# Performance work log

Measured on AMD Instinct MI355X. Metric: run time of the kernel, lower is better.

The kernel has to match this reference:

```python
import math
import jax, jax.numpy as jnp
import numpy as np

HIDDEN = 1024
N_HEADS = 16
HEAD = HIDDEN // N_HEADS
B = 2
L = 2048
STRIDE = 128
EXPR = 8
MAXPOS = 2048


def _checkpoint(wi):
    if wi % STRIDE == 0 and wi != 0:
        return wi - EXPR
    return (wi // STRIDE) * STRIDE + STRIDE - EXPR


def _subset_summaries(absolute_max):
    ci = _checkpoint(0)
    s = set()
    while ci <= absolute_max - 1:
        s |= set(range(ci, min(ci + EXPR + 1, absolute_max)))
        ci = _checkpoint(ci + STRIDE)
    return s


def build_sparse_mask(n, bidirectional=True):
    # Faithful numpy port of prepare_sparse_mask: -1e4 everywhere, 0 at allowed positions.
    mask = np.full((n, n), -10000.0, dtype=np.float32)
    global_summaries = _subset_summaries(n) if bidirectional else set()
    for i in range(n):
        absolute_max = n if bidirectional else i + 1
        rounded = ((i + STRIDE) // STRIDE) * STRIDE
        if i % STRIDE == 0 and i != 0:
            s1 = set(range(i - STRIDE, min(absolute_max, i + 1)))
        else:
            s1 = set(range(max(0, rounded - STRIDE), min(absolute_max, rounded + 1)))
        s2 = set() if bidirectional else _subset_summaries(absolute_max)
        idx = sorted(s1 | s2 | global_summaries)
        mask[i, idx] = 0.0
    return mask


def setup_inputs() -> dict:
    key = jax.random.key(0)
    ks = jax.random.split(key, 8)
    s = 1.0 / math.sqrt(HIDDEN)
    inp = {
        "hidden_states": jax.random.normal(ks[0], (B, L, HIDDEN), dtype=jnp.float32),
        "attention_mask": jnp.zeros((B, 1, 1, L), dtype=jnp.float32),
        "Wq": jax.random.normal(ks[1], (HIDDEN, HIDDEN), dtype=jnp.float32) * s,
        "bq": jnp.zeros((HIDDEN,), dtype=jnp.float32),
        "Wk": jax.random.normal(ks[2], (HIDDEN, HIDDEN), dtype=jnp.float32) * s,
        "bk": jnp.zeros((HIDDEN,), dtype=jnp.float32),
        "Wv": jax.random.normal(ks[3], (HIDDEN, HIDDEN), dtype=jnp.float32) * s,
        "bv": jnp.zeros((HIDDEN,), dtype=jnp.float32),
        "sparse_mask": jnp.asarray(build_sparse_mask(MAXPOS)[:L, :L]),
    }
    return inp


def _split_heads(x):  # [B, L, H] -> [B, nH, L, hd]
    b, l, _ = x.shape
    return x.reshape(b, l, N_HEADS, HEAD).transpose(0, 2, 1, 3)


def reference(hidden_states, attention_mask, Wq, bq, Wk, bk, Wv, bv, sparse_mask):
    q = _split_heads(hidden_states @ Wq + bq)
    k = _split_heads(hidden_states @ Wk + bk)
    v = _split_heads(hidden_states @ Wv + bv)
    scores = jnp.einsum("bhqd,bhkd->bhqk", q, k) / math.sqrt(HEAD)
    scores = scores + sparse_mask  # [L,L] broadcasts over [B,nH,L,L]
    scores = jnp.clip(scores, -10000.0, 10000.0)
    scores = scores + attention_mask
    probs = jax.nn.softmax(scores.astype(jnp.float32), axis=-1).astype(scores.dtype)
    # dropout prob = 0.0 -> identity
    ctx = jnp.einsum("bhqk,bhkd->bhqd", probs, v)
    return ctx.transpose(0, 2, 1, 3).reshape(hidden_states.shape[0], -1, HIDDEN)
```

## Files before the change

kernel.cpp:

```cpp
#include <hip/hip_runtime.h>

#define HID 1024
#define NH 16
#define HD 64
#define BB 2
#define LL 2048
#define GC 143
#define GP 192
#define AMT_PER_B 2240

typedef __attribute__((ext_vector_type(8))) __bf16 bf16x8;
typedef __attribute__((ext_vector_type(4))) float f32x4;
typedef __attribute__((ext_vector_type(4))) int i32x4;
typedef __attribute__((ext_vector_type(2))) unsigned long long u64x2;

__device__ __forceinline__ void gload_lds16(const void* g, void* l) {
  __builtin_amdgcn_global_load_lds((const __attribute__((address_space(1))) void*)g,
                                   (__attribute__((address_space(3))) void*)l, 16, 0, 0);
}

__device__ __forceinline__ unsigned int cvtpk(float lo, float hi) {
  unsigned int r;
  asm("v_cvt_pk_bf16_f32 %0, %1, %2" : "=v"(r) : "v"(lo), "v"(hi));
  return r;
}

__device__ __forceinline__ bf16x8 vfrag(const char* vbase, int r, int gA, int gB,
                                        int half) {
  unsigned long long lo =
      *(const unsigned long long*)(vbase + r * 128 + ((gA ^ (r & 7)) << 4) + half);
  unsigned long long hi =
      *(const unsigned long long*)(vbase + r * 128 + ((gB ^ (r & 7)) << 4) + half);
  u64x2 u;
  u[0] = lo;
  u[1] = hi;
  return __builtin_bit_cast(bf16x8, u);
}

__global__ __launch_bounds__(256) void prep_kernel(
    const float* __restrict__ hs, __bf16* __restrict__ hsb,
    const float* __restrict__ Wq, const float* __restrict__ Wk,
    const float* __restrict__ Wv, __bf16* __restrict__ wtb,
    const float* __restrict__ amask, unsigned int* __restrict__ zbase,
    float* __restrict__ amt) {
  int bx = blockIdx.x;
  int t = threadIdx.x;
  if (bx < 2048) {
    int i = bx * 256 + t;
    const float4* src = (const float4*)hs;
    float4 a = src[2 * i], b = src[2 * i + 1];
    bf16x8 v;
    v[0] = (__bf16)a.x; v[1] = (__bf16)a.y; v[2] = (__bf16)a.z; v[3] = (__bf16)a.w;
    v[4] = (__bf16)b.x; v[5] = (__bf16)b.y; v[6] = (__bf16)b.z; v[7] = (__bf16)b.w;
    ((bf16x8*)hsb)[i] = v;
  } else if (bx < 2048 + 768) {
    int z3 = bx - 2048;
    int kt = z3 & 15, nt = (z3 >> 4) & 15, z = z3 >> 8;
    const float* w = (z == 0) ? Wq : (z == 1) ? Wk : Wv;
    __bf16* dst = wtb + (size_t)z * HID * HID;
    __shared__ __bf16 tile[64][66];
    int cr = t & 63, rr = t >> 6;
#pragma unroll
    for (int it = 0; it < 16; it++) {
      int r = it * 4 + rr;
      tile[cr][r] = (__bf16)w[(size_t)(kt * 64 + r) * HID + nt * 64 + cr];
    }
    __syncthreads();
#pragma unroll
    for (int it = 0; it < 16; it++) {
      int r = it * 4 + rr;
      dst[(size_t)(nt * 64 + r) * HID + kt * 64 + cr] = tile[r][cr];
    }
  } else if (bx < 2048 + 768 + 1536) {
    int i = (bx - 2816) * 256 + t;
    zbase[i] = 0u;
  } else {
    int idx = (bx - 4352) * 256 + t;
    if (idx < BB * AMT_PER_B) {
      int b = idx / AMT_PER_B, r = idx % AMT_PER_B;
      float val;
      if (r < GP) {
        int k = r / 9, j = r - 9 * k;
        val = (r < GC) ? (amask[b * LL + 120 + 128 * k + j] - 20.f) : -1e5f;
      } else {
        int r2 = r - GP;
        int w = r2 >> 7, off = r2 & 127;
        bool gcol = (off >= 120) || (off == 0 && w != 0);
        val = gcol ? -1e5f : (amask[b * LL + w * 128 + off] - 20.f);
      }
      amt[idx] = val;
    }
  }
}

__global__ __launch_bounds__(256, 2) void qkv_gemm_kernel(
    const __bf16* __restrict__ hsb, const __bf16* __restrict__ wtb,
    const float* __restrict__ bq, const float* __restrict__ bk,
    const float* __restrict__ bv, __bf16* __restrict__ qb,
    __bf16* __restrict__ kkb, __bf16* __restrict__ vtb,
    __bf16* __restrict__ kgb, __bf16* __restrict__ vgb) {
  int nt = blockIdx.x, mt = blockIdx.y, which = blockIdx.z;
  const __bf16* wt = wtb + (size_t)which * HID * HID;
  const float* bias = (which == 0) ? bq : (which == 1) ? bk : bv;

  __shared__ __bf16 a_lds[128 * 64];
  __shared__ __bf16 b_lds[128 * 64];

  int tid = threadIdx.x;
  int wave = tid >> 6, lane = tid & 63;
  int wm = wave >> 1, wn = wave & 1;
  int lrow = lane & 15, lgr = lane >> 4, g = lane & 7;

  f32x4 acc[4][4];
#pragma unroll
  for (int i = 0; i < 4; i++)
#pragma unroll
    for (int j = 0; j < 4; j++) acc[i][j] = f32x4{0.f, 0.f, 0.f, 0.f};

  for (int kk = 0; kk < HID; kk += 64) {
#pragma unroll
    for (int i = 0; i < 4; i++) {
      int r = (wave * 4 + i) * 8 + (lane >> 3);
      int gs = (g ^ (r & 7)) * 8;
      gload_lds16(hsb + (size_t)(mt * 128 + r) * HID + kk + gs,
                  &a_lds[(wave * 4 + i) * 512]);
      gload_lds16(wt + (size_t)(nt * 128 + r) * HID + kk + gs,
                  &b_lds[(wave * 4 + i) * 512]);
    }
    __syncthreads();
#pragma unroll
    for (int kf = 0; kf < 2; kf++) {
      bf16x8 af[4], bfr[4];
#pragma unroll
      for (int mr = 0; mr < 4; mr++) {
        int row = wm * 64 + mr * 16 + lrow;
        af[mr] = *(const bf16x8*)((const char*)a_lds + row * 128 +
                                  ((kf * 64 + lgr * 16) ^ ((row & 7) << 4)));
      }
#pragma unroll
      for (int nr = 0; nr < 4; nr++) {
        int row = wn * 64 + nr * 16 + lrow;
        bfr[nr] = *(const bf16x8*)((const char*)b_lds + row * 128 +
                                   ((kf * 64 + lgr * 16) ^ ((row & 7) << 4)));
      }
#pragma unroll
      for (int mr = 0; mr < 4; mr++)
#pragma unroll
        for (int nr = 0; nr < 4; nr++)
          acc[mr][nr] = __builtin_amdgcn_mfma_f32_16x16x32_bf16(
              af[mr], bfr[nr], acc[mr][nr], 0, 0, 0);
    }
    __syncthreads();
  }

#pragma unroll
  for (int nr = 0; nr < 4; nr++) {
    int n = nt * 128 + wn * 64 + nr * 16 + lrow;
    float bsv = bias[n];
    int hh = n >> 6, d = n & 63;
#pragma unroll
    for (int mr = 0; mr < 4; mr++) {
#pragma unroll
      for (int reg = 0; reg < 4; reg++) {
        int m = mt * 128 + wm * 64 + mr * 16 + lgr * 4 + reg;
        int bidx = m >> 11, l = m & 2047;
        float val = acc[mr][nr][reg] + bsv;
        int c7 = l & 127;
        bool isg = (c7 >= 120) || (c7 == 0 && l != 0);
        int cidx = (c7 >= 120) ? ((l >> 7) * 9 + (c7 - 120)) : (((l >> 7) - 1) * 9 + 8);
        if (which == 0) {
          val *= 0.125f;
          qb[((size_t)(bidx * NH + hh) * LL + l) * HD + d] = (__bf16)val;
        } else if (which == 1) {
          __bf16 bv16 = (__bf16)val;
          kkb[((size_t)(bidx * NH + hh) * LL + l) * HD + d] = bv16;
          if (isg) kgb[((size_t)(bidx * NH + hh) * GP + cidx) * HD + d] = bv16;
        } else {
          __bf16 bv16 = (__bf16)val;
          vtb[((size_t)(bidx * NH + hh) * HD + d) * LL + l] = bv16;
          if (isg) vgb[((size_t)(bidx * NH + hh) * HD + d) * GP + cidx] = bv16;
        }
      }
    }
  }
}

__global__ __launch_bounds__(256, 4) void attn_kernel(
    const __bf16* __restrict__ qb, const __bf16* __restrict__ kkb,
    const __bf16* __restrict__ vtb, const __bf16* __restrict__ kgb,
    const __bf16* __restrict__ vgb, const float* __restrict__ amt,
    float* __restrict__ out) {
  __shared__ __bf16 kbuf[2][64 * 64];
  __shared__ __bf16 vbuf[2][64 * 64];

  int qt = blockIdx.x, hh = blockIdx.y, b = blockIdx.z;
  int tid = threadIdx.x, wave = tid >> 6, lane = tid & 63;
  int lrow = lane & 15, lgr = lane >> 4, g = lane & 7;

  const __bf16* qbh = qb + (size_t)(b * NH + hh) * LL * HD;
  const __bf16* kbh = kkb + (size_t)(b * NH + hh) * LL * HD;
  const __bf16* vth = vtb + (size_t)(b * NH + hh) * HD * LL;
  const __bf16* kgh = kgb + (size_t)(b * NH + hh) * GP * HD;
  const __bf16* vgh = vgb + (size_t)(b * NH + hh) * HD * GP;

  int shift = (qt == 16) ? 0 : 1;
  int qt2 = (qt == 16) ? 0 : qt;
  int W = qt2 * 128;
  const float* amt_b = amt + b * AMT_PER_B;
  const float* amt_l = amt_b + GP + qt2 * 128;

  int qrowA = qt2 * 128 + shift + wave * 32 + lrow;
  int qrowB = qrowA + 16;
  int qldA = (qrowA > LL - 1) ? (LL - 1) : qrowA;
  int qldB = (qrowB > LL - 1) ? (LL - 1) : qrowB;
  bf16x8 qA0 = *(const bf16x8*)(qbh + (size_t)qldA * HD + lgr * 8);
  bf16x8 qA1 = *(const bf16x8*)(qbh + (size_t)qldA * HD + 32 + lgr * 8);
  bf16x8 qB0 = *(const bf16x8*)(qbh + (size_t)qldB * HD + lgr * 8);
  bf16x8 qB1 = *(const bf16x8*)(qbh + (size_t)qldB * HD + 32 + lgr * 8);

  int g0 = lgr >> 1, half = (lgr & 1) * 8;

  float lA = 0.f, lB = 0.f;
  f32x4 oA[4], oB[4];
#pragma unroll
  for (int i = 0; i < 4; i++) {
    oA[i] = f32x4{0.f, 0.f, 0.f, 0.f};
    oB[i] = f32x4{0.f, 0.f, 0.f, 0.f};
  }

#define STAGE(IT, BI)                                                     \
  do {                                                                    \
    const __bf16 *ks_, *vs_;                                              \
    int vst_;                                                             \
    if ((IT) < 3) {                                                       \
      ks_ = kgh + (size_t)((IT)*64) * HD;                                 \
      vs_ = vgh + (IT)*64;                                                \
      vst_ = GP;                                                          \
    } else {                                                              \
      int cb_ = W + ((IT)-3) * 64;                                        \
      ks_ = kbh + (size_t)cb_ * HD;                                       \
      vs_ = vth + cb_;                                                    \
      vst_ = LL;                                                          \
    }                                                                     \
    _Pragma("unroll")                                                     \
    for (int i_ = 0; i_ < 2; i_++) {                                      \
      int r_ = (wave * 2 + i_) * 8 + (lane >> 3);                         \
      int gs_ = (g ^ (r_ & 7)) * 8;                                       \
      gload_lds16(ks_ + (size_t)r_ * HD + gs_, &kbuf[BI][(wave * 2 + i_) * 512]); \
      gload_lds16(vs_ + (size_t)r_ * vst_ + gs_, &vbuf[BI][(wave * 2 + i_) * 512]); \
    }                                                                     \
  } while (0)

  STAGE(0, 0);
  __syncthreads();

#pragma unroll
  for (int it = 0; it < 5; it++) {
    int cur = it & 1;
    if (it < 4) STAGE(it + 1, cur ^ 1);

    const __bf16* k_lds = kbuf[cur];
    const char* v_ldsc = (const char*)vbuf[cur];

    const float* abase = (it < 3) ? (amt_b + it * 64) : (amt_l + (it - 3) * 64);
    f32x4 ad[4];
#pragma unroll
    for (int nr = 0; nr < 4; nr++)
      ad[nr] = *(const f32x4*)(abase + nr * 16 + lgr * 4);

    f32x4 sA[4], sB[4];
    __builtin_amdgcn_s_setprio(1);
#pragma unroll
    for (int nr = 0; nr < 4; nr++) {
      int row = nr * 16 + lrow;
      bf16x8 kf0 = *(const bf16x8*)((const char*)k_lds + row * 128 +
                                    ((lgr * 16) ^ ((row & 7) << 4)));
      bf16x8 kf1 = *(const bf16x8*)((const char*)k_lds + row * 128 +
                                    ((64 + lgr * 16) ^ ((row & 7) << 4)));
      f32x4 zA = f32x4{0.f, 0.f, 0.f, 0.f};
      zA = __builtin_amdgcn_mfma_f32_16x16x32_bf16(kf0, qA0, zA, 0, 0, 0);
      zA = __builtin_amdgcn_mfma_f32_16x16x32_bf16(kf1, qA1, zA, 0, 0, 0);
      sA[nr] = zA;
      f32x4 zB = f32x4{0.f, 0.f, 0.f, 0.f};
      zB = __builtin_amdgcn_mfma_f32_16x16x32_bf16(kf0, qB0, zB, 0, 0, 0);
      zB = __builtin_amdgcn_mfma_f32_16x16x32_bf16(kf1, qB1, zB, 0, 0, 0);
      sB[nr] = zB;
    }
    __builtin_amdgcn_s_setprio(0);

#pragma unroll
    for (int nr = 0; nr < 4; nr++) {
#pragma unroll
      for (int reg = 0; reg < 4; reg++) {
        float vA = fminf(fmaxf(sA[nr][reg], -10000.f), 10000.f) + ad[nr][reg];
        float pA = __expf(vA);
        sA[nr][reg] = pA;
        lA += pA;
        float vB = fminf(fmaxf(sB[nr][reg], -10000.f), 10000.f) + ad[nr][reg];
        float pB = __expf(vB);
        sB[nr][reg] = pB;
        lB += pB;
      }
    }

    i32x4 wA0, wA1, wB0, wB1;
    wA0[0] = (int)cvtpk(sA[0][0], sA[0][1]);
    wA0[1] = (int)cvtpk(sA[0][2], sA[0][3]);
    wA0[2] = (int)cvtpk(sA[1][0], sA[1][1]);
    wA0[3] = (int)cvtpk(sA[1][2], sA[1][3]);
    wA1[0] = (int)cvtpk(sA[2][0], sA[2][1]);
    wA1[1] = (int)cvtpk(sA[2][2], sA[2][3]);
    wA1[2] = (int)cvtpk(sA[3][0], sA[3][1]);
    wA1[3] = (int)cvtpk(sA[3][2], sA[3][3]);
    wB0[0] = (int)cvtpk(sB[0][0], sB[0][1]);
    wB0[1] = (int)cvtpk(sB[0][2], sB[0][3]);
    wB0[2] = (int)cvtpk(sB[1][0], sB[1][1]);
    wB0[3] = (int)cvtpk(sB[1][2], sB[1][3]);
    wB1[0] = (int)cvtpk(sB[2][0], sB[2][1]);
    wB1[1] = (int)cvtpk(sB[2][2], sB[2][3]);
    wB1[2] = (int)cvtpk(sB[3][0], sB[3][1]);
    wB1[3] = (int)cvtpk(sB[3][2], sB[3][3]);
    bf16x8 pbA0 = __builtin_bit_cast(bf16x8, wA0);
    bf16x8 pbA1 = __builtin_bit_cast(bf16x8, wA1);
    bf16x8 pbB0 = __builtin_bit_cast(bf16x8, wB0);
    bf16x8 pbB1 = __builtin_bit_cast(bf16x8, wB1);

    __builtin_amdgcn_s_setprio(1);
#pragma unroll
    for (int nd = 0; nd < 4; nd++) {
      int row = nd * 16 + lrow;
      bf16x8 va0 = vfrag(v_ldsc, row, g0, 2 + g0, half);
      bf16x8 va1 = vfrag(v_ldsc, row, 4 + g0, 6 + g0, half);
      oA[nd] = __builtin_amdgcn_mfma_f32_16x16x32_bf16(va0, pbA0, oA[nd], 0, 0, 0);
      oA[nd] = __builtin_amdgcn_mfma_f32_16x16x32_bf16(va1, pbA1, oA[nd], 0, 0, 0);
      oB[nd] = __builtin_amdgcn_mfma_f32_16x16x32_bf16(va0, pbB0, oB[nd], 0, 0, 0);
      oB[nd] = __builtin_amdgcn_mfma_f32_16x16x32_bf16(va1, pbB1, oB[nd], 0, 0, 0);
    }
    __builtin_amdgcn_s_setprio(0);
    if (it < 4) __syncthreads();
  }
#undef STAGE

  lA += __shfl_xor(lA, 16);
  lA += __shfl_xor(lA, 32);
  lB += __shfl_xor(lB, 16);
  lB += __shfl_xor(lB, 32);
  float rlA = 1.f / lA, rlB = 1.f / lB;

  if (qrowA < LL) {
    float* obase = out + ((size_t)b * LL + qrowA) * HID + hh * HD + lgr * 4;
#pragma unroll
    for (int nd = 0; nd < 4; nd++) {
      float4 ov;
      ov.x = oA[nd][0] * rlA;
      ov.y = oA[nd][1] * rlA;
      ov.z = oA[nd][2] * rlA;
      ov.w = oA[nd][3] * rlA;
      *(float4*)(obase + nd * 16) = ov;
    }
  }
  if (qrowB < LL) {
    float* obase = out + ((size_t)b * LL + qrowB) * HID + hh * HD + lgr * 4;
#pragma unroll
    for (int nd = 0; nd < 4; nd++) {
      float4 ov;
      ov.x = oB[nd][0] * rlB;
      ov.y = oB[nd][1] * rlB;
      ov.z = oB[nd][2] * rlB;
      ov.w = oB[nd][3] * rlB;
      *(float4*)(obase + nd * 16) = ov;
    }
  }
}

extern "C" void kernel_launch(void* const* d_in, const int* in_sizes, int n_in,
                              void* d_out, int out_size, void* d_ws, size_t ws_size,
                              hipStream_t stream) {
  (void)in_sizes; (void)n_in; (void)out_size; (void)ws_size;
  const float* hs = (const float*)d_in[0];
  const float* amask = (const float*)d_in[1];
  const float* Wq = (const float*)d_in[2];
  const float* bq = (const float*)d_in[3];
  const float* Wk = (const float*)d_in[4];
  const float* bk = (const float*)d_in[5];
  const float* Wv = (const float*)d_in[6];
  const float* bv = (const float*)d_in[7];
  float* out = (float*)d_out;

  char* ws = (char*)d_ws;
  __bf16* hsb = (__bf16*)(ws);
  __bf16* wtb = (__bf16*)(ws + 8388608);
  __bf16* qb  = (__bf16*)(ws + 14680064);
  __bf16* kb  = (__bf16*)(ws + 23068672);
  __bf16* vtb = (__bf16*)(ws + 31457280);
  __bf16* kgb = (__bf16*)(ws + 39845888);
  __bf16* vgb = (__bf16*)(ws + 40632320);
  float*  amt = (float*)(ws + 41418752);

  hipLaunchKernelGGL(prep_kernel, dim3(4370), dim3(256), 0, stream,
                     hs, hsb, Wq, Wk, Wv, wtb, amask, (unsigned int*)kgb, amt);
  hipLaunchKernelGGL(qkv_gemm_kernel, dim3(8, 32, 3), dim3(256), 0, stream,
                     hsb, wtb, bq, bk, bv, qb, kb, vtb, kgb, vgb);
  hipLaunchKernelGGL(attn_kernel, dim3(17, NH, BB), dim3(256), 0, stream,
                     qb, kb, vtb, kgb, vgb, amt, out);
}
```

Before: 69.45 us.

## Rewrite QKV GEMM with 256x256 tiles, 8 waves and double-buffered LDS prefetch

Result: slower. 95.89 us (+38.1%).

```diff
diff --git a/kernel.cpp b/kernel.cpp
--- a/kernel.cpp
+++ b/kernel.cpp
@@ -93,7 +93,7 @@
   }
 }
 
-__global__ __launch_bounds__(256, 2) void qkv_gemm_kernel(
+__global__ __launch_bounds__(512, 2) void qkv_gemm_kernel(
     const __bf16* __restrict__ hsb, const __bf16* __restrict__ wtb,
     const float* __restrict__ bq, const float* __restrict__ bk,
     const float* __restrict__ bv, __bf16* __restrict__ qb,
@@ -103,68 +103,118 @@
   const __bf16* wt = wtb + (size_t)which * HID * HID;
   const float* bias = (which == 0) ? bq : (which == 1) ? bk : bv;
 
-  __shared__ __bf16 a_lds[128 * 64];
-  __shared__ __bf16 b_lds[128 * 64];
+  __shared__ __bf16 Ab[2][256 * 64];
+  __shared__ __bf16 Bb[2][256 * 64];
 
   int tid = threadIdx.x;
   int wave = tid >> 6, lane = tid & 63;
-  int wm = wave >> 1, wn = wave & 1;
-  int lrow = lane & 15, lgr = lane >> 4, g = lane & 7;
-
-  f32x4 acc[4][4];
-#pragma unroll
-  for (int i = 0; i < 4; i++)
+  int wm = wave >> 2, wn = wave & 3;
+  int lrow = lane & 15, lgr = lane >> 4;
+
+  int srow_base = wave * 8 + (lane >> 3);
+  int sg = lane & 7;
+
+#define STAGE_A(KT, I)                                                        \
+  do {                                                                        \
+    int r_ = (I)*64 + srow_base;                                              \
+    int gs_ = (sg ^ (r_ & 7)) * 8;                                            \
+    gload_lds16(hsb + (size_t)(mt * 256 + r_) * HID + (KT)*64 + gs_,          \
+                &Ab[(KT)&1][((I)*64 + wave * 8) * 64]);                       \
+  } while (0)
+#define STAGE_B(KT, I)                                                        \
+  do {                                                                        \
+    int r_ = (I)*64 + srow_base;                                              \
+    int gs_ = (sg ^ (r_ & 7)) * 8;                                            \
+    gload_lds16(wt + (size_t)(nt * 256 + r_) * HID + (KT)*64 + gs_,           \
+                &Bb[(KT)&1][((I)*64 + wave * 8) * 64]);                       \
+  } while (0)
+
+  f32x4 acc[8][4];
+#pragma unroll
+  for (int i = 0; i < 8; i++)
 #pragma unroll
     for (int j = 0; j < 4; j++) acc[i][j] = f32x4{0.f, 0.f, 0.f, 0.f};
 
-  for (int kk = 0; kk < HID; kk += 64) {
-#pragma unroll
-    for (int i = 0; i < 4; i++) {
-      int r = (wave * 4 + i) * 8 + (lane >> 3);
-      int gs = (g ^ (r & 7)) * 8;
-      gload_lds16(hsb + (size_t)(mt * 128 + r) * HID + kk + gs,
-                  &a_lds[(wave * 4 + i) * 512]);
-      gload_lds16(wt + (size_t)(nt * 128 + r) * HID + kk + gs,
-                  &b_lds[(wave * 4 + i) * 512]);
-    }
-    __syncthreads();
-#pragma unroll
-    for (int kf = 0; kf < 2; kf++) {
-      bf16x8 af[4], bfr[4];
-#pragma unroll
-      for (int mr = 0; mr < 4; mr++) {
-        int row = wm * 64 + mr * 16 + lrow;
-        af[mr] = *(const bf16x8*)((const char*)a_lds + row * 128 +
-                                  ((kf * 64 + lgr * 16) ^ ((row & 7) << 4)));
-      }
-#pragma unroll
-      for (int nr = 0; nr < 4; nr++) {
-        int row = wn * 64 + nr * 16 + lrow;
-        bfr[nr] = *(const bf16x8*)((const char*)b_lds + row * 128 +
-                                   ((kf * 64 + lgr * 16) ^ ((row & 7) << 4)));
-      }
-#pragma unroll
-      for (int mr = 0; mr < 4; mr++)
-#pragma unroll
-        for (int nr = 0; nr < 4; nr++)
-          acc[mr][nr] = __builtin_amdgcn_mfma_f32_16x16x32_bf16(
-              af[mr], bfr[nr], acc[mr][nr], 0, 0, 0);
-    }
-    __syncthreads();
-  }
-
-#pragma unroll
-  for (int nr = 0; nr < 4; nr++) {
-    int n = nt * 128 + wn * 64 + nr * 16 + lrow;
+#pragma unroll
+  for (int i = 0; i < 4; i++) {
+    STAGE_A(0, i);
+    STAGE_B(0, i);
+  }
+  asm volatile("s_waitcnt vmcnt(0)" ::: "memory");
+  __builtin_amdgcn_s_barrier();
+
+  for (int t = 0; t < 16; t++) {
+    const char* Ap = (const char*)&Ab[t & 1][0];
+    const char* Bp = (const char*)&Bb[t & 1][0];
+
+    bf16x8 bfr[4][2];
+#pragma unroll
+    for (int n = 0; n < 4; n++) {
+      int row = wn * 64 + n * 16 + lrow;
+#pragma unroll
+      for (int kf = 0; kf < 2; kf++)
+        bfr[n][kf] = *(const bf16x8*)(Bp + row * 128 +
+                                      ((kf * 64 + lgr * 16) ^ ((row & 7) << 4)));
+    }
+
+#pragma unroll
+    for (int p = 0; p < 4; p++) {
+      bf16x8 af[2][2];
+#pragma unroll
+      for (int j = 0; j < 2; j++) {
+        int row = wm * 128 + (2 * p + j) * 16 + lrow;
+#pragma unroll
+        for (int kf = 0; kf < 2; kf++)
+          af[j][kf] = *(const bf16x8*)(Ap + row * 128 +
+                                       ((kf * 64 + lgr * 16) ^ ((row & 7) << 4)));
+      }
+      if (p == 0 && t < 15) {
+        STAGE_A(t + 1, 1);
+        STAGE_A(t + 1, 3);
+      }
+      if (p == 1 && t < 15) {
+        STAGE_B(t + 1, 0);
+        STAGE_B(t + 1, 1);
+        STAGE_B(t + 1, 2);
+        STAGE_B(t + 1, 3);
+        STAGE_A(t + 1, 0);
+        STAGE_A(t + 1, 2);
+      }
+      __builtin_amdgcn_s_barrier();
+      __builtin_amdgcn_s_setprio(1);
+#pragma unroll
+      for (int j = 0; j < 2; j++)
+#pragma unroll
+        for (int n = 0; n < 4; n++) {
+          acc[2 * p + j][n] = __builtin_amdgcn_mfma_f32_16x16x32_bf16(
+              af[j][0], bfr[n][0], acc[2 * p + j][n], 0, 0, 0);
+          acc[2 * p + j][n] = __builtin_amdgcn_mfma_f32_16x16x32_bf16(
+              af[j][1], bfr[n][1], acc[2 * p + j][n], 0, 0, 0);
+        }
+      __builtin_amdgcn_s_setprio(0);
+      __builtin_amdgcn_s_barrier();
+    }
+
+    if (t < 15) {
+      asm volatile("s_waitcnt vmcnt(0)" ::: "memory");
+      __builtin_amdgcn_s_barrier();
+    }
+  }
+#undef STAGE_A
+#undef STAGE_B
+
+#pragma unroll
+  for (int nfr = 0; nfr < 4; nfr++) {
+    int n = nt * 256 + wn * 64 + nfr * 16 + lrow;
     float bsv = bias[n];
     int hh = n >> 6, d = n & 63;
 #pragma unroll
-    for (int mr = 0; mr < 4; mr++) {
+    for (int mfr = 0; mfr < 8; mfr++) {
 #pragma unroll
       for (int reg = 0; reg < 4; reg++) {
-        int m = mt * 128 + wm * 64 + mr * 16 + lgr * 4 + reg;
+        int m = mt * 256 + wm * 128 + mfr * 16 + lgr * 4 + reg;
         int bidx = m >> 11, l = m & 2047;
-        float val = acc[mr][nr][reg] + bsv;
+        float val = acc[mfr][nfr][reg] + bsv;
         int c7 = l & 127;
         bool isg = (c7 >= 120) || (c7 == 0 && l != 0);
         int cidx = (c7 >= 120) ? ((l >> 7) * 9 + (c7 - 120)) : (((l >> 7) - 1) * 9 + 8);
@@ -399,7 +449,7 @@
 
   hipLaunchKernelGGL(prep_kernel, dim3(4370), dim3(256), 0, stream,
                      hs, hsb, Wq, Wk, Wv, wtb, amask, (unsigned int*)kgb, amt);
-  hipLaunchKernelGGL(qkv_gemm_kernel, dim3(8, 32, 3), dim3(256), 0, stream,
+  hipLaunchKernelGGL(qkv_gemm_kernel, dim3(4, 16, 3), dim3(512), 0, stream,
                      hsb, wtb, bq, bk, bv, qb, kb, vtb, kgb, vgb);
   hipLaunchKernelGGL(attn_kernel, dim3(17, NH, BB), dim3(256), 0, stream,
                      qb, kb, vtb, kgb, vgb, amt, out);
```
